# Kernel optimization log

Measured on AMD Instinct MI355X. Metric: run time of the kernel, lower is better.

## Reference

```python
import jax, jax.numpy as jnp
import numpy as np

H, KD, VD, KNN = 8, 64, 64, 128
D, FC, N, S = 512, 2048, 4, 1024
GW_DEC, GW_ENC = 0.5, 0.5
EPS = 1e-5
SCALE = float(np.sqrt(KD))


def _layer_norm(x):
    # nn.LayerNorm(out_dim, eps=1e-5, elementwise_affine=False)
    m = jnp.mean(x, -1, keepdims=True)
    v = jnp.var(x, -1, keepdims=True)
    return (x - m) * jax.lax.rsqrt(v + EPS)


def _mha(x, Wk, bk, Wv, bv, Wo, bo, att_graph, gw, mask, Wq=None, bq=None, q_in=None):
    # x: [N,S,D]; per-head projections stacked: Wk [H,D,Kd], Wv [H,D,Vd]
    key = jnp.einsum('nsd,hdk->hnsk', x, Wk) + bk[:, None, None, :]
    value = jnp.einsum('nsd,hdv->hnsv', x, Wv) + bv[:, None, None, :]
    if q_in is None:
        query = key  # self-attention: query = key (as in the torch code)
    else:
        query = jnp.einsum('nqd,hdk->hnqk', q_in, Wq) + bq[:, None, None, :]
    # broadcast-mul-sum in torch == batched matmul
    att = jnp.einsum('hnqk,hnsk->hnqs', query, key) / SCALE  # [H,N,Q,S]
    if mask:
        qlen, slen = att.shape[-2], att.shape[-1]
        causal = jnp.arange(slen)[None, :] <= jnp.arange(qlen)[:, None]
        att = jnp.where(causal, att, -jnp.inf)
    # knn sparsification: keep top-KNN per row, rest -> -inf (equiv to topk+scatter for distinct values)
    thresh = jax.lax.top_k(att, KNN)[0][..., -1:]
    att = jnp.where(att >= thresh, att, -jnp.inf)
    att = jax.nn.softmax(att, axis=-1)
    # blend with precomputed (softmaxed) graph attention
    att = gw * att_graph + (1.0 - gw) * att
    ctx = jnp.einsum('hnqs,hnsv->hnqv', att, value)  # [H,N,Q,Vd]
    ctx = jnp.transpose(ctx, (1, 2, 0, 3)).reshape(ctx.shape[1], ctx.shape[2], H * VD)
    return ctx @ Wo + bo


def setup_inputs() -> dict:
    key = jax.random.key(0)
    ks = jax.random.split(key, 22)
    p = lambda k, shp: (0.02 * jax.random.normal(k, shp)).astype(jnp.float32)
    return {
        'z': jax.random.normal(ks[0], (N, S, D), jnp.float32),
        'y': jax.random.normal(ks[1], (N, S, D), jnp.float32),
        'graph_dec': jax.random.normal(ks[2], (S, S), jnp.float32),
        'graph_enc': jax.random.normal(ks[3], (S, S), jnp.float32),
        'dec_Wk': p(ks[4], (H, D, KD)), 'dec_bk': p(ks[5], (H, KD)),
        'dec_Wv': p(ks[6], (H, D, VD)), 'dec_bv': p(ks[7], (H, VD)),
        'dec_Wo': p(ks[8], (H * VD, D)), 'dec_bo': p(ks[9], (D,)),
        'enc_Wk': p(ks[10], (H, D, KD)), 'enc_bk': p(ks[11], (H, KD)),
        'enc_Wq': p(ks[12], (H, D, KD)), 'enc_bq': p(ks[13], (H, KD)),
        'enc_Wv': p(ks[14], (H, D, VD)), 'enc_bv': p(ks[15], (H, VD)),
        'enc_Wo': p(ks[16], (H * VD, D)), 'enc_bo': p(ks[17], (D,)),
        'fc_W1': p(ks[18], (D, FC)), 'fc_b1': p(ks[19], (FC,)),
        'fc_W2': p(ks[20], (FC, D)), 'fc_b2': p(ks[21], (D,)),
    }


def reference(z, y, graph_dec, graph_enc, dec_Wk, dec_bk, dec_Wv, dec_bv, dec_Wo, dec_bo, enc_Wk, enc_bk, enc_Wq, enc_bq, enc_Wv, enc_bv, enc_Wo, enc_bo, fc_W1, fc_b1, fc_W2, fc_b2):
    # graphs are row-softmaxed at construction time in the torch module
    gdec = jax.nn.softmax(graph_dec, axis=-1)
    genc = jax.nn.softmax(graph_enc, axis=-1)
    # 1) masked decoder self-attention on y
    h = _mha(y, dec_Wk, dec_bk, dec_Wv, dec_bv, dec_Wo, dec_bo, gdec, GW_DEC, True)
    h = _layer_norm(h + y)
    # 2) encoder-decoder attention: keys/values from z, query from h via query_keys (query_key=True)
    h2 = _mha(z, enc_Wk, enc_bk, enc_Wv, enc_bv, enc_Wo, enc_bo, genc, GW_ENC, False, enc_Wq, enc_bq, h)
    h2 = _layer_norm(h2 + h)
    # 3) two-layer MLP
    h3 = jax.nn.relu(h2 @ fc_W1 + fc_b1) @ fc_W2 + fc_b2
    return _layer_norm(h3 + h2)
```

## Files before the change

kernel.cpp:

```cpp
#include <hip/hip_runtime.h>
#include <stdint.h>

typedef short short8 __attribute__((ext_vector_type(8)));
typedef short short4v __attribute__((ext_vector_type(4)));
typedef float floatx4 __attribute__((ext_vector_type(4)));
typedef unsigned uint4v __attribute__((ext_vector_type(4)));

#define H_  8
#define NB_ 4
#define S_  1024
#define D_  512
#define KD_ 64

__device__ __forceinline__ short f2bf(float f){
    unsigned u = __builtin_bit_cast(unsigned, f);
    u += 0x7fffu + ((u>>16)&1u);
    return (short)(u>>16);
}
__device__ __forceinline__ float wred_addf(float x){
    #pragma unroll
    for(int o=32;o>0;o>>=1) x += __shfl_xor(x,o,64);
    return x;
}
__device__ __forceinline__ float wred_maxf(float x){
    #pragma unroll
    for(int o=32;o>0;o>>=1) x = fmaxf(x,__shfl_xor(x,o,64));
    return x;
}
__device__ __forceinline__ unsigned umaxu(unsigned a, unsigned b){ return a>b?a:b; }

template<int CTRL, int RMASK, int BC>
__device__ __forceinline__ unsigned dppu(unsigned x){
    return (unsigned)__builtin_amdgcn_update_dpp(0, (int)x, CTRL, RMASK, 0xf, BC);
}
__device__ __forceinline__ unsigned wsum_dpp_u(unsigned x){
    x += dppu<0x111,0xf,1>(x);
    x += dppu<0x112,0xf,1>(x);
    x += dppu<0x114,0xf,1>(x);
    x += dppu<0x118,0xf,1>(x);
    x += dppu<0x142,0xa,0>(x);
    x += dppu<0x143,0xc,0>(x);
    return (unsigned)__builtin_amdgcn_readlane((int)x, 63);
}
__device__ __forceinline__ unsigned wmax_dpp_u(unsigned x){
    x = umaxu(x, dppu<0x111,0xf,1>(x));
    x = umaxu(x, dppu<0x112,0xf,1>(x));
    x = umaxu(x, dppu<0x114,0xf,1>(x));
    x = umaxu(x, dppu<0x118,0xf,1>(x));
    x = umaxu(x, dppu<0x142,0xa,0>(x));
    x = umaxu(x, dppu<0x143,0xc,0>(x));
    return (unsigned)__builtin_amdgcn_readlane((int)x, 63);
}
__device__ __forceinline__ float addu_f(float a, unsigned b){
    return a + __builtin_bit_cast(float, b);
}
__device__ __forceinline__ float wsum_dpp_f(float x){
    x = addu_f(x, dppu<0x111,0xf,1>(__builtin_bit_cast(unsigned,x)));
    x = addu_f(x, dppu<0x112,0xf,1>(__builtin_bit_cast(unsigned,x)));
    x = addu_f(x, dppu<0x114,0xf,1>(__builtin_bit_cast(unsigned,x)));
    x = addu_f(x, dppu<0x118,0xf,1>(__builtin_bit_cast(unsigned,x)));
    x = addu_f(x, dppu<0x142,0xa,0>(__builtin_bit_cast(unsigned,x)));
    x = addu_f(x, dppu<0x143,0xc,0>(__builtin_bit_cast(unsigned,x)));
    return __builtin_bit_cast(float, (unsigned)__builtin_amdgcn_readlane((int)__builtin_bit_cast(unsigned, x), 63));
}
__device__ __forceinline__ unsigned cvt_pk_bf16(float a, float b){
    unsigned r;
    asm("v_cvt_pk_bf16_f32 %0, %1, %2" : "=v"(r) : "v"(a), "v"(b));
    return r;
}

__global__ __launch_bounds__(256) void cvt2_kernel(const float* __restrict__ a, const float* __restrict__ b,
                                                   short* __restrict__ oa, short* __restrict__ ob){
    const float* in = blockIdx.y ? b : a;
    short* out = blockIdx.y ? ob : oa;
    int i = (blockIdx.x*256 + threadIdx.x)*4;
    floatx4 v = *(const floatx4*)(in + i);
    short4v r;
    #pragma unroll
    for(int j=0;j<4;j++) r[j] = f2bf(v[j]);
    *(short4v*)(out + i) = r;
}

__global__ __launch_bounds__(256) void wtrans5_kernel(
    const float* __restrict__ dWk, const float* __restrict__ dWv,
    const float* __restrict__ eWk, const float* __restrict__ eWv, const float* __restrict__ eWq,
    short* __restrict__ wKVd, short* __restrict__ wKVe, short* __restrict__ wQet)
{
    __shared__ float t[32][33];
    int zz = blockIdx.z; int w = zz>>3, h = zz&7;
    const float* src; short* dst;
    if(w==0){ src = dWk + h*32768; dst = wKVd + h*65536; }
    else if(w==1){ src = dWv + h*32768; dst = wKVd + h*65536 + 32768; }
    else if(w==2){ src = eWk + h*32768; dst = wKVe + h*65536; }
    else if(w==3){ src = eWv + h*32768; dst = wKVe + h*65536 + 32768; }
    else { src = eWq + h*32768; dst = wQet + h*32768; }
    const int R = 512, C = 64;
    int c0 = blockIdx.x*32, r0 = blockIdx.y*32;
    int tid = threadIdx.x;
    int r = tid>>3, cq = (tid&7)*4;
    #pragma unroll
    for(int i=0;i<4;i++) t[r][cq+i] = src[(r0+r)*C + c0+cq+i];
    __syncthreads();
    int c = tid>>3, rq = (tid&7)*4;
    #pragma unroll
    for(int i=0;i<4;i++) dst[(c0+c)*R + r0+rq+i] = f2bf(t[rq+i][c]);
}

__global__ __launch_bounds__(256) void wtrans4_kernel(
    const float* __restrict__ dWo, const float* __restrict__ eWo,
    const float* __restrict__ W1, const float* __restrict__ W2,
    short* __restrict__ oWod, short* __restrict__ oWoe,
    short* __restrict__ oW1, short* __restrict__ oW2)
{
    __shared__ float t[32][33];
    int id = blockIdx.x;
    const float* src; short* dst; int R, C, c0, r0;
    if(id < 512){
        src = (id<256)? dWo : eWo; dst = (id<256)? oWod : oWoe;
        int tt = id & 255; R = 512; C = 512;
        c0 = (tt&15)*32; r0 = (tt>>4)*32;
    } else if(id < 1536){
        src = W1; dst = oW1; int tt = id - 512; R = 512; C = 2048;
        c0 = (tt&63)*32; r0 = (tt>>6)*32;
    } else {
        src = W2; dst = oW2; int tt = id - 1536; R = 2048; C = 512;
        c0 = (tt&15)*32; r0 = (tt>>4)*32;
    }
    int tid = threadIdx.x;
    int r = tid>>3, cq = (tid&7)*4;
    #pragma unroll
    for(int i=0;i<4;i++) t[r][cq+i] = src[(long)(r0+r)*C + c0+cq+i];
    __syncthreads();
    int c = tid>>3, rq = (tid&7)*4;
    #pragma unroll
    for(int i=0;i<4;i++) dst[(long)(c0+c)*R + r0+rq+i] = f2bf(t[rq+i][c]);
}

__global__ __launch_bounds__(256) void graph_softmax_kernel(const float* __restrict__ g0,
                                                            const float* __restrict__ g1,
                                                            short* __restrict__ o0,
                                                            short* __restrict__ o1){
    int row = blockIdx.x;
    const float* g = blockIdx.y ? g1 : g0;
    short* o = blockIdx.y ? o1 : o0;
    const float* gr = g + (long)row*S_;
    short* orow = o + (long)row*S_;
    int tid = threadIdx.x, wave = tid>>6, lane = tid&63;
    __shared__ float red[8];
    float v[4]; float mx = -3.0e38f;
    #pragma unroll
    for(int i=0;i<4;i++){ v[i] = gr[tid + 256*i]; mx = fmaxf(mx, v[i]); }
    mx = wred_maxf(mx);
    if(lane==0) red[wave] = mx;
    __syncthreads();
    mx = fmaxf(fmaxf(red[0],red[1]), fmaxf(red[2],red[3]));
    float s = 0.f;
    #pragma unroll
    for(int i=0;i<4;i++){ v[i] = __expf(v[i]-mx); s += v[i]; }
    s = wred_addf(s);
    if(lane==0) red[4+wave] = s;
    __syncthreads();
    s = red[4]+red[5]+red[6]+red[7];
    float inv = 0.5f/s;
    #pragma unroll
    for(int i=0;i<4;i++) orow[tid + 256*i] = f2bf(v[i]*inv);
}

template<int KV>
__global__ __launch_bounds__(256) void gemm_proj_kernel(
    const short* __restrict__ A, const short* __restrict__ Bt,
    const float* __restrict__ b1, const float* __restrict__ b2,
    short* __restrict__ o1, short* __restrict__ o2)
{
    constexpr int TN = KV ? 128 : 64;
    constexpr int NI = TN/32;
    __shared__ short As[64*32];
    __shared__ short Bs[TN*32];
    int z = blockIdx.z;
    int m0 = blockIdx.x*64;
    const short* Bb = Bt + (long)z*(TN*512);
    int tid = threadIdx.x, wave = tid>>6, lane = tid&63, quad = lane>>4, nl = lane&15;
    int wm = (wave&1)*32, wn = (wave>>1)*(TN/2);
    floatx4 acc[2][NI];
    #pragma unroll
    for(int i=0;i<2;i++)
        #pragma unroll
        for(int j=0;j<NI;j++) acc[i][j] = (floatx4){0.f,0.f,0.f,0.f};
    int r = tid>>2, c = (tid&3)*8;
    for(int k0=0;k0<512;k0+=32){
        __syncthreads();
        __builtin_amdgcn_global_load_lds(
            (const __attribute__((address_space(1))) unsigned*)(A + (long)(m0 + r)*512 + k0 + c),
            (__attribute__((address_space(3))) unsigned*)((char*)As + wave*1024), 16, 0, 0);
        #pragma unroll
        for(int i=0;i<TN/64;i++)
            __builtin_amdgcn_global_load_lds(
                (const __attribute__((address_space(1))) unsigned*)(Bb + (long)(r + i*64)*512 + k0 + c),
                (__attribute__((address_space(3))) unsigned*)((char*)Bs + i*4096 + wave*1024), 16, 0, 0);
        __syncthreads();
        short8 af[2], bfr[NI];
        #pragma unroll
        for(int i=0;i<2;i++) af[i] = *(const short8*)(As + (wm + i*16 + nl)*32 + quad*8);
        #pragma unroll
        for(int j=0;j<NI;j++) bfr[j] = *(const short8*)(Bs + (wn + j*16 + nl)*32 + quad*8);
        #pragma unroll
        for(int i=0;i<2;i++)
            #pragma unroll
            for(int j=0;j<NI;j++)
                acc[i][j] = __builtin_amdgcn_mfma_f32_16x16x32_bf16(af[i],bfr[j],acc[i][j],0,0,0);
    }
    #pragma unroll
    for(int j=0;j<NI;j++){
        int n = wn + j*16 + nl;
        float bv = (KV && n >= 64) ? b2[z*64 + n - 64] : b1[z*64 + n];
        #pragma unroll
        for(int i=0;i<2;i++){
            #pragma unroll
            for(int rr=0;rr<4;rr++){
                int m = m0 + wm + i*16 + quad*4 + rr;
                float v = acc[i][j][rr] + bv;
                long zb = (long)(z*NB_ + (m>>10));
                if(KV && n >= 64) o2[ (zb*KD_ + (n-64))*S_ + (m&1023) ] = f2bf(v);
                else              o1[ (zb*S_ + (m&1023))*KD_ + n ] = f2bf(v);
            }
        }
    }
}

template<int TM, int TN, int OUTBF, int RELU>
__global__ __launch_bounds__(256) void gemm_big_kernel(
    const short* __restrict__ A, const short* __restrict__ Bt, const float* __restrict__ bias,
    void* __restrict__ out, int M, int N, int K)
{
    __shared__ short As[TM*32];
    __shared__ short Bs[TN*32];
    int m0 = blockIdx.x*TM, n0 = blockIdx.y*TN;
    int tid = threadIdx.x, wave = tid>>6, lane = tid&63, quad = lane>>4, nl = lane&15;
    constexpr int MI = TM/32, NI = TN/32;
    int wm = (wave&1)*(TM/2), wn = (wave>>1)*(TN/2);
    floatx4 acc[MI][NI];
    #pragma unroll
    for(int i=0;i<MI;i++)
        #pragma unroll
        for(int j=0;j<NI;j++) acc[i][j] = (floatx4){0.f,0.f,0.f,0.f};

    int r = tid>>2, c = (tid&3)*8;
    for(int k0=0;k0<K;k0+=32){
        __syncthreads();
        #pragma unroll
        for(int i=0;i<TM/64;i++)
            __builtin_amdgcn_global_load_lds(
                (const __attribute__((address_space(1))) unsigned*)(A + (long)(m0 + r + i*64)*K + k0 + c),
                (__attribute__((address_space(3))) unsigned*)((char*)As + i*4096 + wave*1024),
                16, 0, 0);
        #pragma unroll
        for(int i=0;i<TN/64;i++)
            __builtin_amdgcn_global_load_lds(
                (const __attribute__((address_space(1))) unsigned*)(Bt + (long)(n0 + r + i*64)*K + k0 + c),
                (__attribute__((address_space(3))) unsigned*)((char*)Bs + i*4096 + wave*1024),
                16, 0, 0);
        __syncthreads();
        short8 af[MI], bfr[NI];
        #pragma unroll
        for(int i=0;i<MI;i++) af[i] = *(const short8*)(As + (wm + i*16 + nl)*32 + quad*8);
        #pragma unroll
        for(int j=0;j<NI;j++) bfr[j] = *(const short8*)(Bs + (wn + j*16 + nl)*32 + quad*8);
        #pragma unroll
        for(int i=0;i<MI;i++)
            #pragma unroll
            for(int j=0;j<NI;j++)
                acc[i][j] = __builtin_amdgcn_mfma_f32_16x16x32_bf16(af[i],bfr[j],acc[i][j],0,0,0);
    }
    #pragma unroll
    for(int j=0;j<NI;j++){
        int n = n0 + wn + j*16 + nl;
        float bv = bias[n];
        #pragma unroll
        for(int i=0;i<MI;i++){
            #pragma unroll
            for(int rr=0;rr<4;rr++){
                int m = m0 + wm + i*16 + quad*4 + rr;
                float v = acc[i][j][rr] + bv;
                if(RELU) v = fmaxf(v, 0.f);
                if(OUTBF) ((short*)out)[(long)m*N + n] = f2bf(v);
                else      ((float*)out)[(long)m*N + n] = v;
            }
        }
    }
}

__global__ __launch_bounds__(512,6) void attn_kernel(
    const short* __restrict__ Qb, const short* __restrict__ Kb, const short* __restrict__ Vt,
    const short* __restrict__ graph, short* __restrict__ ctx, int causal)
{
    __shared__ short attb[16*1024];
    __shared__ float pbuf[16*68];
    int hn = blockIdx.x, qt = blockIdx.y;
    int h = hn>>2, n = hn&3;
    int q0 = qt*16;
    int tid=threadIdx.x, wave=tid>>6, lane=tid&63, quad=lane>>4, nl=lane&15;

    if(causal){
        uint4v fv = (uint4v){0xff80ff80u,0xff80ff80u,0xff80ff80u,0xff80ff80u};
        #pragma unroll
        for(int i=0;i<4;i++) *(uint4v*)((char*)attb + tid*16 + i*8192) = fv;
        __syncthreads();
    }

    const short* Qp = Qb + ((long)hn*S_ + q0 + nl)*KD_ + quad*8;
    short8 aq0 = *(const short8*)(Qp);
    short8 aq1 = *(const short8*)(Qp + 32);
    const short* Kp = Kb + (long)hn*S_*KD_;
    int stmax = causal ? qt : 63;
    for(int st=wave; st<=stmax; st+=8){
        const short* kp = Kp + (st*16 + nl)*KD_ + quad*8;
        short8 b0 = *(const short8*)(kp);
        short8 b1 = *(const short8*)(kp + 32);
        floatx4 cc = (floatx4){0.f,0.f,0.f,0.f};
        cc = __builtin_amdgcn_mfma_f32_16x16x32_bf16(aq0,b0,cc,0,0,0);
        cc = __builtin_amdgcn_mfma_f32_16x16x32_bf16(aq1,b1,cc,0,0,0);
        int s = st*16 + nl;
        #pragma unroll
        for(int rr=0;rr<4;rr++){
            int q = quad*4 + rr;
            short val = f2bf(cc[rr]*0.125f);
            if(causal && s > q0 + q) val = (short)0xff80;
            attb[q*1024 + ((s + 8*q)&1023)] = val;
        }
    }
    __syncthreads();

    #pragma unroll 1
    for(int rp=0; rp<2; ++rp){
        int q = wave*2 + rp;
        int qg = q0 + q;
        short* rowp = attb + q*1024;
        int sb = lane*16;
        int p0 = (sb + 8*q) & 1023;
        uint4v u0 = *(const uint4v*)(rowp + p0);
        uint4v u1 = *(const uint4v*)(rowp + ((p0+8)&1023));
        unsigned pr[8];
        #pragma unroll
        for(int i=0;i<4;i++){ pr[i] = u0[i]; pr[4+i] = u1[i]; }
        unsigned kv[16];
        #pragma unroll
        for(int i=0;i<8;i++){
            unsigned u = pr[i];
            unsigned kp = u ^ (0x80008000u + ((u>>15)&0x00010001u)*0x7fffu);
            kv[2*i]   = kp & 0xffffu;
            kv[2*i+1] = kp >> 16;
        }
        unsigned a0 = umaxu(kv[0],kv[1]),  a1 = umaxu(kv[2],kv[3]);
        unsigned a2 = umaxu(kv[4],kv[5]),  a3 = umaxu(kv[6],kv[7]);
        unsigned a4 = umaxu(kv[8],kv[9]),  a5 = umaxu(kv[10],kv[11]);
        unsigned a6 = umaxu(kv[12],kv[13]),a7 = umaxu(kv[14],kv[15]);
        unsigned mk = umaxu(umaxu(umaxu(a0,a1),umaxu(a2,a3)), umaxu(umaxu(a4,a5),umaxu(a6,a7)));
        unsigned mks = wmax_dpp_u(mk);
        unsigned lo = 0u, hi = mks + 1u;
        while(hi - lo > 1u){
            unsigned mid = (lo + hi) >> 1;
            unsigned c = 0u;
            #pragma unroll
            for(int j=0;j<16;j++) c += (unsigned)(kv[j] >= mid);
            unsigned tot = wsum_dpp_u(c);
            if(tot >= 128u) lo = mid; else hi = mid;
        }
        unsigned uo = (mks & 0x8000u) ? ((mks & 0x7fffu)<<16) : ((~mks)<<16);
        float mxf = __builtin_bit_cast(float, uo);
        float ev[16]; float sm = 0.f;
        #pragma unroll
        for(int i=0;i<8;i++){
            float f0 = __builtin_bit_cast(float, pr[i] << 16);
            float f1 = __builtin_bit_cast(float, pr[i] & 0xffff0000u);
            float e0 = __expf(f0 - mxf);
            float e1 = __expf(f1 - mxf);
            e0 = (kv[2*i]   >= lo) ? e0 : 0.f;
            e1 = (kv[2*i+1] >= lo) ? e1 : 0.f;
            ev[2*i] = e0; ev[2*i+1] = e1;
            sm += e0 + e1;
        }
        sm = wsum_dpp_f(sm);
        float inv = 0.5f / sm;
        const short* grow = graph + (long)qg*1024 + sb;
        uint4v g0 = *(const uint4v*)(grow);
        uint4v g1 = *(const uint4v*)(grow + 8);
        unsigned gp[8];
        #pragma unroll
        for(int i=0;i<4;i++){ gp[i] = g0[i]; gp[4+i] = g1[i]; }
        uint4v w0, w1;
        #pragma unroll
        for(int i=0;i<8;i++){
            float gl = __builtin_bit_cast(float, gp[i] << 16);
            float gh = __builtin_bit_cast(float, gp[i] & 0xffff0000u);
            float r0 = fmaf(ev[2*i],   inv, gl);
            float r1 = fmaf(ev[2*i+1], inv, gh);
            unsigned pk = cvt_pk_bf16(r0, r1);
            if(i<4) w0[i] = pk; else w1[i-4] = pk;
        }
        *(uint4v*)(rowp + p0) = w0;
        *(uint4v*)(rowp + ((p0+8)&1023)) = w1;
    }
    __syncthreads();

    int vh = wave & 3, sh = wave >> 2;
    int v0 = vh*16;
    const short* Vp = Vt + ((long)hn*KD_ + v0 + nl)*S_;
    floatx4 o4 = (floatx4){0.f,0.f,0.f,0.f};
    int arow = nl;
    int sbase = sh*512;
    for(int s0=sbase; s0<sbase+512; s0+=32){
        int cs = (s0 + quad*8 + 8*arow) & 1023;
        short8 ap = *(const short8*)(attb + arow*1024 + cs);
        short8 bv = *(const short8*)(Vp + s0 + quad*8);
        o4 = __builtin_amdgcn_mfma_f32_16x16x32_bf16(ap,bv,o4,0,0,0);
    }
    if(sh==1){
        #pragma unroll
        for(int rr=0;rr<4;rr++) pbuf[(quad*4+rr)*68 + v0 + nl] = o4[rr];
    }
    __syncthreads();
    if(sh==0){
        #pragma unroll
        for(int rr=0;rr<4;rr++){
            int q = quad*4 + rr;
            float v = o4[rr] + pbuf[q*68 + v0 + nl];
            ctx[ ((long)(n*S_ + q0 + q))*512 + h*KD_ + v0 + nl ] = f2bf(v);
        }
    }
}

__global__ __launch_bounds__(256) void ln_kernel(const float* __restrict__ x, const float* __restrict__ res,
                                                 float* __restrict__ outf, short* __restrict__ outb){
    long row = blockIdx.x;
    const float* xr = x + row*D_;
    const float* rr = res + row*D_;
    int tid = threadIdx.x, wave = tid>>6, lane = tid&63;
    float t0 = xr[tid] + rr[tid];
    float t1 = xr[tid+256] + rr[tid+256];
    float s = t0 + t1, s2 = t0*t0 + t1*t1;
    __shared__ float red[8];
    s = wred_addf(s); s2 = wred_addf(s2);
    if(lane==0){ red[wave] = s; red[4+wave] = s2; }
    __syncthreads();
    s  = red[0]+red[1]+red[2]+red[3];
    s2 = red[4]+red[5]+red[6]+red[7];
    float mean = s*(1.f/512.f);
    float var = s2*(1.f/512.f) - mean*mean;
    float rs = rsqrtf(var + 1e-5f);
    float o0 = (t0-mean)*rs, o1 = (t1-mean)*rs;
    if(outf){ outf[row*D_+tid] = o0; outf[row*D_+tid+256] = o1; }
    if(outb){ outb[row*D_+tid] = f2bf(o0); outb[row*D_+tid+256] = f2bf(o1); }
}

extern "C" void kernel_launch(void* const* d_in, const int* in_sizes, int n_in,
                              void* d_out, int out_size, void* d_ws, size_t ws_size,
                              hipStream_t stream)
{
    const float* z         = (const float*)d_in[0];
    const float* y         = (const float*)d_in[1];
    const float* graph_dec = (const float*)d_in[2];
    const float* graph_enc = (const float*)d_in[3];
    const float* dec_Wk = (const float*)d_in[4];  const float* dec_bk = (const float*)d_in[5];
    const float* dec_Wv = (const float*)d_in[6];  const float* dec_bv = (const float*)d_in[7];
    const float* dec_Wo = (const float*)d_in[8];  const float* dec_bo = (const float*)d_in[9];
    const float* enc_Wk = (const float*)d_in[10]; const float* enc_bk = (const float*)d_in[11];
    const float* enc_Wq = (const float*)d_in[12]; const float* enc_bq = (const float*)d_in[13];
    const float* enc_Wv = (const float*)d_in[14]; const float* enc_bv = (const float*)d_in[15];
    const float* enc_Wo = (const float*)d_in[16]; const float* enc_bo = (const float*)d_in[17];
    const float* fc_W1  = (const float*)d_in[18]; const float* fc_b1  = (const float*)d_in[19];
    const float* fc_W2  = (const float*)d_in[20]; const float* fc_b2  = (const float*)d_in[21];

    char* ws = (char*)d_ws;
    short* gdec  = (short*)(ws + 0x0000000);
    short* genc  = (short*)(ws + 0x0400000);
    short* y_bf  = (short*)(ws + 0x0800000);
    short* z_bf  = (short*)(ws + 0x0C00000);
    short* Kdec  = (short*)(ws + 0x1000000);
    short* Vtdec = (short*)(ws + 0x1400000);
    short* Kenc  = (short*)(ws + 0x1800000);
    short* Vtenc = (short*)(ws + 0x1C00000);
    short* Qenc  = (short*)(ws + 0x2000000);
    short* ctx   = (short*)(ws + 0x2400000);
    float* tmp   = (float*)(ws + 0x2800000);
    float* hbuf  = (float*)(ws + 0x3000000);
    short* h_bf  = (short*)(ws + 0x3800000);
    float* h2    = (float*)(ws + 0x3C00000);
    short* h2_bf = (short*)(ws + 0x4400000);
    short* fc1   = (short*)(ws + 0x4800000);
    short* wKVd  = (short*)(ws + 0x5800000);
    short* wKVe  = (short*)(ws + 0x5900000);
    short* wQet  = (short*)(ws + 0x5A00000);
    short* wOdt  = (short*)(ws + 0x5A80000);
    short* wOet  = (short*)(ws + 0x5B00000);
    short* wF1t  = (short*)(ws + 0x5B80000);
    short* wF2t  = (short*)(ws + 0x5D80000);
    float* outp  = (float*)d_out;

    dim3 B(256);
    wtrans5_kernel<<<dim3(2,16,40),B,0,stream>>>(dec_Wk, dec_Wv, enc_Wk, enc_Wv, enc_Wq, wKVd, wKVe, wQet);
    wtrans4_kernel<<<dim3(2560),B,0,stream>>>(dec_Wo, enc_Wo, fc_W1, fc_W2, wOdt, wOet, wF1t, wF2t);
    cvt2_kernel<<<dim3(2048,2),B,0,stream>>>(y, z, y_bf, z_bf);
    graph_softmax_kernel<<<dim3(1024,2),B,0,stream>>>(graph_dec, graph_enc, gdec, genc);
    gemm_proj_kernel<1><<<dim3(64,1,8),B,0,stream>>>(y_bf, wKVd, dec_bk, dec_bv, Kdec, Vtdec);
    attn_kernel<<<dim3(32,64),dim3(512),0,stream>>>(Kdec, Kdec, Vtdec, gdec, ctx, 1);
    gemm_big_kernel<64,128,0,0><<<dim3(64,4),B,0,stream>>>(ctx, wOdt, dec_bo, tmp, 4096, 512, 512);
    ln_kernel<<<dim3(4096),B,0,stream>>>(tmp, y, hbuf, h_bf);
    gemm_proj_kernel<1><<<dim3(64,1,8),B,0,stream>>>(z_bf, wKVe, enc_bk, enc_bv, Kenc, Vtenc);
    gemm_proj_kernel<0><<<dim3(64,1,8),B,0,stream>>>(h_bf, wQet, enc_bq, (const float*)0, Qenc, (short*)0);
    attn_kernel<<<dim3(32,64),dim3(512),0,stream>>>(Qenc, Kenc, Vtenc, genc, ctx, 0);
    gemm_big_kernel<64,128,0,0><<<dim3(64,4),B,0,stream>>>(ctx, wOet, enc_bo, tmp, 4096, 512, 512);
    ln_kernel<<<dim3(4096),B,0,stream>>>(tmp, hbuf, h2, h2_bf);
    gemm_big_kernel<128,128,1,1><<<dim3(32,16),B,0,stream>>>(h2_bf, wF1t, fc_b1, fc1, 4096, 2048, 512);
    gemm_big_kernel<64,128,0,0><<<dim3(64,4),B,0,stream>>>(fc1, wF2t, fc_b2, tmp, 4096, 512, 2048);
    ln_kernel<<<dim3(4096),B,0,stream>>>(tmp, h2, outp, (short*)0);
}
```

Measured before the change: 394.4 us.

## Interleave two rows' top-k bisection and tighten lower bound via per-lane second max

```diff
diff --git a/kernel.cpp b/kernel.cpp
--- a/kernel.cpp
+++ b/kernel.cpp
@@ -28,10 +28,15 @@
     return x;
 }
 __device__ __forceinline__ unsigned umaxu(unsigned a, unsigned b){ return a>b?a:b; }
+__device__ __forceinline__ unsigned uminu(unsigned a, unsigned b){ return a<b?a:b; }
 
 template<int CTRL, int RMASK, int BC>
 __device__ __forceinline__ unsigned dppu(unsigned x){
     return (unsigned)__builtin_amdgcn_update_dpp(0, (int)x, CTRL, RMASK, 0xf, BC);
+}
+template<int CTRL, int RMASK>
+__device__ __forceinline__ unsigned dppu_m1(unsigned x){
+    return (unsigned)__builtin_amdgcn_update_dpp((int)0xFFFFFFFF, (int)x, CTRL, RMASK, 0xf, 0);
 }
 __device__ __forceinline__ unsigned wsum_dpp_u(unsigned x){
     x += dppu<0x111,0xf,1>(x);
@@ -49,6 +54,15 @@
     x = umaxu(x, dppu<0x118,0xf,1>(x));
     x = umaxu(x, dppu<0x142,0xa,0>(x));
     x = umaxu(x, dppu<0x143,0xc,0>(x));
+    return (unsigned)__builtin_amdgcn_readlane((int)x, 63);
+}
+__device__ __forceinline__ unsigned wmin_dpp_u(unsigned x){
+    x = uminu(x, dppu_m1<0x111,0xf>(x));
+    x = uminu(x, dppu_m1<0x112,0xf>(x));
+    x = uminu(x, dppu_m1<0x114,0xf>(x));
+    x = uminu(x, dppu_m1<0x118,0xf>(x));
+    x = uminu(x, dppu_m1<0x142,0xa>(x));
+    x = uminu(x, dppu_m1<0x143,0xc>(x));
     return (unsigned)__builtin_amdgcn_readlane((int)x, 63);
 }
 __device__ __forceinline__ float addu_f(float a, unsigned b){
@@ -330,75 +344,136 @@
     }
     __syncthreads();
 
-    #pragma unroll 1
-    for(int rp=0; rp<2; ++rp){
-        int q = wave*2 + rp;
-        int qg = q0 + q;
-        short* rowp = attb + q*1024;
+    {
+        int qA = wave*2, qB = qA + 1;
+        short* rowA = attb + qA*1024;
+        short* rowB = attb + qB*1024;
         int sb = lane*16;
-        int p0 = (sb + 8*q) & 1023;
-        uint4v u0 = *(const uint4v*)(rowp + p0);
-        uint4v u1 = *(const uint4v*)(rowp + ((p0+8)&1023));
-        unsigned pr[8];
-        #pragma unroll
-        for(int i=0;i<4;i++){ pr[i] = u0[i]; pr[4+i] = u1[i]; }
-        unsigned kv[16];
+        int pA = (sb + 8*qA) & 1023;
+        int pB = (sb + 8*qB) & 1023;
+
+        const short* gAp = graph + (long)(q0+qA)*1024 + sb;
+        const short* gBp = graph + (long)(q0+qB)*1024 + sb;
+        uint4v gA0 = *(const uint4v*)(gAp);
+        uint4v gA1 = *(const uint4v*)(gAp + 8);
+        uint4v gB0 = *(const uint4v*)(gBp);
+        uint4v gB1 = *(const uint4v*)(gBp + 8);
+
+        uint4v uA0 = *(const uint4v*)(rowA + pA);
+        uint4v uA1 = *(const uint4v*)(rowA + ((pA+8)&1023));
+        uint4v uB0 = *(const uint4v*)(rowB + pB);
+        uint4v uB1 = *(const uint4v*)(rowB + ((pB+8)&1023));
+
+        unsigned kvA[16], kvB[16];
+        #pragma unroll
+        for(int i=0;i<4;i++){
+            unsigned u, kp;
+            u = uA0[i]; kp = u ^ (0x80008000u + ((u>>15)&0x00010001u)*0x7fffu);
+            kvA[2*i] = kp & 0xffffu; kvA[2*i+1] = kp >> 16;
+            u = uA1[i]; kp = u ^ (0x80008000u + ((u>>15)&0x00010001u)*0x7fffu);
+            kvA[8+2*i] = kp & 0xffffu; kvA[8+2*i+1] = kp >> 16;
+            u = uB0[i]; kp = u ^ (0x80008000u + ((u>>15)&0x00010001u)*0x7fffu);
+            kvB[2*i] = kp & 0xffffu; kvB[2*i+1] = kp >> 16;
+            u = uB1[i]; kp = u ^ (0x80008000u + ((u>>15)&0x00010001u)*0x7fffu);
+            kvB[8+2*i] = kp & 0xffffu; kvB[8+2*i+1] = kp >> 16;
+        }
+
+        unsigned m1A[8], m2A[8], m1B[8], m2B[8];
         #pragma unroll
         for(int i=0;i<8;i++){
-            unsigned u = pr[i];
-            unsigned kp = u ^ (0x80008000u + ((u>>15)&0x00010001u)*0x7fffu);
-            kv[2*i]   = kp & 0xffffu;
-            kv[2*i+1] = kp >> 16;
-        }
-        unsigned a0 = umaxu(kv[0],kv[1]),  a1 = umaxu(kv[2],kv[3]);
-        unsigned a2 = umaxu(kv[4],kv[5]),  a3 = umaxu(kv[6],kv[7]);
-        unsigned a4 = umaxu(kv[8],kv[9]),  a5 = umaxu(kv[10],kv[11]);
-        unsigned a6 = umaxu(kv[12],kv[13]),a7 = umaxu(kv[14],kv[15]);
-        unsigned mk = umaxu(umaxu(umaxu(a0,a1),umaxu(a2,a3)), umaxu(umaxu(a4,a5),umaxu(a6,a7)));
-        unsigned mks = wmax_dpp_u(mk);
-        unsigned lo = 0u, hi = mks + 1u;
-        while(hi - lo > 1u){
-            unsigned mid = (lo + hi) >> 1;
-            unsigned c = 0u;
-            #pragma unroll
-            for(int j=0;j<16;j++) c += (unsigned)(kv[j] >= mid);
-            unsigned tot = wsum_dpp_u(c);
-            if(tot >= 128u) lo = mid; else hi = mid;
-        }
-        unsigned uo = (mks & 0x8000u) ? ((mks & 0x7fffu)<<16) : ((~mks)<<16);
-        float mxf = __builtin_bit_cast(float, uo);
-        float ev[16]; float sm = 0.f;
-        #pragma unroll
-        for(int i=0;i<8;i++){
-            float f0 = __builtin_bit_cast(float, pr[i] << 16);
-            float f1 = __builtin_bit_cast(float, pr[i] & 0xffff0000u);
-            float e0 = __expf(f0 - mxf);
-            float e1 = __expf(f1 - mxf);
-            e0 = (kv[2*i]   >= lo) ? e0 : 0.f;
-            e1 = (kv[2*i+1] >= lo) ? e1 : 0.f;
-            ev[2*i] = e0; ev[2*i+1] = e1;
-            sm += e0 + e1;
-        }
-        sm = wsum_dpp_f(sm);
-        float inv = 0.5f / sm;
-        const short* grow = graph + (long)qg*1024 + sb;
-        uint4v g0 = *(const uint4v*)(grow);
-        uint4v g1 = *(const uint4v*)(grow + 8);
-        unsigned gp[8];
-        #pragma unroll
-        for(int i=0;i<4;i++){ gp[i] = g0[i]; gp[4+i] = g1[i]; }
-        uint4v w0, w1;
-        #pragma unroll
-        for(int i=0;i<8;i++){
-            float gl = __builtin_bit_cast(float, gp[i] << 16);
-            float gh = __builtin_bit_cast(float, gp[i] & 0xffff0000u);
-            float r0 = fmaf(ev[2*i],   inv, gl);
-            float r1 = fmaf(ev[2*i+1], inv, gh);
-            unsigned pk = cvt_pk_bf16(r0, r1);
-            if(i<4) w0[i] = pk; else w1[i-4] = pk;
-        }
-        *(uint4v*)(rowp + p0) = w0;
-        *(uint4v*)(rowp + ((p0+8)&1023)) = w1;
+            m1A[i] = umaxu(kvA[2*i], kvA[2*i+1]); m2A[i] = uminu(kvA[2*i], kvA[2*i+1]);
+            m1B[i] = umaxu(kvB[2*i], kvB[2*i+1]); m2B[i] = uminu(kvB[2*i], kvB[2*i+1]);
+        }
+        #pragma unroll
+        for(int st2=8; st2>1; st2>>=1){
+            #pragma unroll
+            for(int i=0;i<8;i++){
+                if(i < st2/2){
+                    unsigned n1 = umaxu(m1A[i], m1A[i+st2/2]);
+                    unsigned n2 = umaxu(uminu(m1A[i], m1A[i+st2/2]), umaxu(m2A[i], m2A[i+st2/2]));
+                    m1A[i]=n1; m2A[i]=n2;
+                    n1 = umaxu(m1B[i], m1B[i+st2/2]);
+                    n2 = umaxu(uminu(m1B[i], m1B[i+st2/2]), umaxu(m2B[i], m2B[i+st2/2]));
+                    m1B[i]=n1; m2B[i]=n2;
+                }
+            }
+        }
+        unsigned mksA = wmax_dpp_u(m1A[0]);
+        unsigned mksB = wmax_dpp_u(m1B[0]);
+        unsigned loA = wmin_dpp_u(m2A[0]), hiA = mksA + 1u;
+        unsigned loB = wmin_dpp_u(m2B[0]), hiB = mksB + 1u;
+
+        while( ((hiA-loA) | (hiB-loB)) != 1u ){
+            unsigned midA = (loA + hiA) >> 1;
+            unsigned midB = (loB + hiB) >> 1;
+            unsigned cA = 0u, cB = 0u;
+            #pragma unroll
+            for(int j=0;j<16;j++){
+                cA += (unsigned)(kvA[j] >= midA);
+                cB += (unsigned)(kvB[j] >= midB);
+            }
+            unsigned tA = wsum_dpp_u(cA);
+            unsigned tB = wsum_dpp_u(cB);
+            if(tA >= 128u) loA = midA; else hiA = midA;
+            if(tB >= 128u) loB = midB; else hiB = midB;
+        }
+
+        {
+            unsigned uo = (mksA & 0x8000u) ? ((mksA & 0x7fffu)<<16) : ((~mksA)<<16);
+            float mxf = __builtin_bit_cast(float, uo);
+            float ev[16]; float sm = 0.f;
+            #pragma unroll
+            for(int j=0;j<16;j++){
+                unsigned k = kvA[j];
+                unsigned ub = (k & 0x8000u) ? (k ^ 0x8000u) : ((~k) & 0xffffu);
+                float f = __builtin_bit_cast(float, ub << 16);
+                float e = __expf(f - mxf);
+                e = (k >= loA) ? e : 0.f;
+                ev[j] = e; sm += e;
+            }
+            sm = wsum_dpp_f(sm);
+            float inv = 0.5f / sm;
+            uint4v w0, w1;
+            #pragma unroll
+            for(int i=0;i<4;i++){
+                float gl0 = __builtin_bit_cast(float, gA0[i] << 16);
+                float gh0 = __builtin_bit_cast(float, gA0[i] & 0xffff0000u);
+                w0[i] = cvt_pk_bf16(fmaf(ev[2*i], inv, gl0), fmaf(ev[2*i+1], inv, gh0));
+                float gl1 = __builtin_bit_cast(float, gA1[i] << 16);
+                float gh1 = __builtin_bit_cast(float, gA1[i] & 0xffff0000u);
+                w1[i] = cvt_pk_bf16(fmaf(ev[8+2*i], inv, gl1), fmaf(ev[8+2*i+1], inv, gh1));
+            }
+            *(uint4v*)(rowA + pA) = w0;
+            *(uint4v*)(rowA + ((pA+8)&1023)) = w1;
+        }
+        {
+            unsigned uo = (mksB & 0x8000u) ? ((mksB & 0x7fffu)<<16) : ((~mksB)<<16);
+            float mxf = __builtin_bit_cast(float, uo);
+            float ev[16]; float sm = 0.f;
+            #pragma unroll
+            for(int j=0;j<16;j++){
+                unsigned k = kvB[j];
+                unsigned ub = (k & 0x8000u) ? (k ^ 0x8000u) : ((~k) & 0xffffu);
+                float f = __builtin_bit_cast(float, ub << 16);
+                float e = __expf(f - mxf);
+                e = (k >= loB) ? e : 0.f;
+                ev[j] = e; sm += e;
+            }
+            sm = wsum_dpp_f(sm);
+            float inv = 0.5f / sm;
+            uint4v w0, w1;
+            #pragma unroll
+            for(int i=0;i<4;i++){
+                float gl0 = __builtin_bit_cast(float, gB0[i] << 16);
+                float gh0 = __builtin_bit_cast(float, gB0[i] & 0xffff0000u);
+                w0[i] = cvt_pk_bf16(fmaf(ev[2*i], inv, gl0), fmaf(ev[2*i+1], inv, gh0));
+                float gl1 = __builtin_bit_cast(float, gB1[i] << 16);
+                float gh1 = __builtin_bit_cast(float, gB1[i] & 0xffff0000u);
+                w1[i] = cvt_pk_bf16(fmaf(ev[8+2*i], inv, gl1), fmaf(ev[8+2*i+1], inv, gh1));
+            }
+            *(uint4v*)(rowB + pB) = w0;
+            *(uint4v*)(rowB + ((pB+8)&1023)) = w1;
+        }
     }
     __syncthreads();
 
```

After: 410.2 us. 4.0% more time.
